# Kernel tuning notes

Hardware: AMD Instinct MI355X
Metric: run time of the kernel (lower is better)

The kernel has to match this reference:

```python
import jax, jax.numpy as jnp
import numpy as np

N_NODES = 100000
N_EDGES = 1600000
DIMS = [1, 20, 40, 60, 80, 100]  # int(k/5*qubo_size) for qubo_size=100


def setup_inputs() -> dict:
    key = jax.random.key(0)
    ks = jax.random.split(key, 16)
    inp = {
        "x": jax.random.normal(ks[0], (N_NODES, 1), dtype=jnp.float32),
        "edge_index": jax.random.randint(ks[1], (2, N_EDGES), 0, N_NODES, dtype=jnp.int64),
        "edge_weights": jax.random.uniform(ks[2], (N_EDGES,), dtype=jnp.float32),
    }
    for i in range(5):
        fan_in, fan_out = DIMS[i], DIMS[i + 1]
        scale = (2.0 / (fan_in + fan_out)) ** 0.5  # glorot-ish
        inp[f"W{i+1}"] = jax.random.normal(ks[3 + 2 * i], (fan_in, fan_out), dtype=jnp.float32) * scale
        inp[f"b{i+1}"] = jnp.zeros((fan_out,), dtype=jnp.float32)
    return inp


def reference(x, edge_index, edge_weights, W1, b1, W2, b2, W3, b3, W4, b4, W5, b5):
    n = x.shape[0]
    src, dst = edge_index[0], edge_index[1]
    # GCN symmetric normalization with self loops (fill value 1.0)
    deg = jax.ops.segment_sum(edge_weights, dst, num_segments=n) + 1.0
    dinv = jnp.where(deg > 0, deg ** -0.5, 0.0)
    norm = dinv[src] * edge_weights * dinv[dst]  # [E]
    self_norm = dinv * dinv                      # [N], self-loop weight 1

    def gcn_layer(h, W, b):
        h = h @ W  # [N, out]
        agg = jax.ops.segment_sum(h[src] * norm[:, None], dst, num_segments=n)
        agg = agg + h * self_norm[:, None]
        return agg + b

    for W, b in ((W1, b1), (W2, b2), (W3, b3), (W4, b4), (W5, b5)):
        x = gcn_layer(x, W, b)
    return jax.nn.relu(x)
```

## Files before the change

### kernel.cpp

```cpp
#include <hip/hip_runtime.h>


#define TBB 1024
#define TBK 512
#define BN 256
#define NBLK 256
#define STAGE 4096
#define CAP 4864

__device__ __forceinline__ void chains_block(
    const float* __restrict__ W1, const float* __restrict__ b1,
    const float* __restrict__ W2, const float* __restrict__ b2,
    const float* __restrict__ W3, const float* __restrict__ b3,
    const float* __restrict__ W4, const float* __restrict__ b4,
    const float* __restrict__ W5, float* __restrict__ coef,
    int* lflag, float (*A)[112], float (*Bm)[112]) {
    int t = threadIdx.x;
    if (t < 20) { A[0][t] = W1[t]; A[1][t] = b1[t]; }
    __syncthreads();
    if (t < 40) {
        for (int c = 0; c < 2; ++c) {
            float acc = 0.f;
            for (int k = 0; k < 20; ++k) acc += A[c][k] * W2[k * 40 + t];
            Bm[c][t] = acc;
        }
        Bm[2][t] = b2[t];
    }
    __syncthreads();
    if (t < 60) {
        for (int c = 0; c < 3; ++c) {
            float acc = 0.f;
            for (int k = 0; k < 40; ++k) acc += Bm[c][k] * W3[k * 60 + t];
            A[c][t] = acc;
        }
        A[3][t] = b3[t];
    }
    __syncthreads();
    if (t < 80) {
        for (int c = 0; c < 4; ++c) {
            float acc = 0.f;
            for (int k = 0; k < 60; ++k) acc += A[c][k] * W4[k * 80 + t];
            Bm[c][t] = acc;
        }
        Bm[4][t] = b4[t];
    }
    __syncthreads();
    if (t < 100) {
        int nz = 0;
        for (int c = 0; c < 5; ++c) {
            float acc = 0.f;
            for (int k = 0; k < 80; ++k) acc += Bm[c][k] * W5[k * 100 + t];
            coef[c * 100 + t] = acc;
            if (c > 0 && acc != 0.0f) nz = 1;
        }
        if (nz) atomicOr(lflag, 1);
    }
}

__global__ __launch_bounds__(TBB) void k_build(const int* __restrict__ src,
                                               const int* __restrict__ dst,
                                               const float* __restrict__ w,
                                               int* __restrict__ gcur,
                                               int2* __restrict__ payload,
                                               const float* __restrict__ W1, const float* __restrict__ b1,
                                               const float* __restrict__ W2, const float* __restrict__ b2,
                                               const float* __restrict__ W3, const float* __restrict__ b3,
                                               const float* __restrict__ W4, const float* __restrict__ b4,
                                               const float* __restrict__ W5, float* __restrict__ coef,
                                               int* __restrict__ uflag,
                                               int E, int B, int chunk) {
    __shared__ int lcur[512];
    __shared__ int lbase[512];
    __shared__ int goff[512];
    __shared__ int2 staged[STAGE];
    __shared__ unsigned short jbuf[STAGE];
    int blk = blockIdx.x, tid = threadIdx.x;
    if (blk == NBLK) {
        float (*A)[112]  = (float (*)[112])staged;
        float (*Bm)[112] = (float (*)[112])((char*)staged + 5 * 112 * 4);
        if (tid == 0) lcur[0] = 0;
        __syncthreads();
        chains_block(W1, b1, W2, b2, W3, b3, W4, b4, W5, coef, &lcur[0], A, Bm);
        __syncthreads();
        if (tid == 0) uflag[0] = lcur[0] ? 0 : 1;
        return;
    }
    int e0 = blk * chunk, e1 = min(E, e0 + chunk);
    for (int sbeg = e0; sbeg < e1; sbeg += STAGE) {
        int send = min(e1, sbeg + STAGE);
        int cnt = send - sbeg;
        if (tid < 512) lcur[tid] = 0;
        __syncthreads();
        int es[4], ed[4]; float ew[4]; int ne = 0;
        for (int i = sbeg + tid; i < send; i += TBB) {
            es[ne] = src[i]; ed[ne] = dst[i]; ew[ne] = w[i]; ++ne;
        }
        for (int k = 0; k < ne; ++k) atomicAdd(&lcur[ed[k] >> 8], 1);
        __syncthreads();
        int myv = (tid < 512) ? lcur[tid] : 0;
        if (tid < B && myv > 0)
            goff[tid] = atomicAdd(&gcur[tid], myv);
        if (tid < 512) lbase[tid] = myv;
        __syncthreads();
        for (int o = 1; o < 512; o <<= 1) {
            int t = (tid >= o && tid < 512) ? lbase[tid - o] : 0;
            __syncthreads();
            if (tid < 512) lbase[tid] += t;
            __syncthreads();
        }
        if (tid < 512) {
            int ex = lbase[tid] - myv;
            lbase[tid] = ex;
            lcur[tid] = ex;
        }
        __syncthreads();
        for (int k = 0; k < ne; ++k) {
            int j = ed[k] >> 8;
            int p = atomicAdd(&lcur[j], 1);
            staged[p] = make_int2(es[k] | ((ed[k] & 255) << 17), __float_as_int(ew[k]));
            jbuf[p] = (unsigned short)j;
        }
        __syncthreads();
        for (int p = tid; p < cnt; p += TBB) {
            int j = jbuf[p];
            int slot = goff[j] + (p - lbase[j]);
            if (slot < CAP) payload[(size_t)j * CAP + slot] = staged[p];
        }
        __syncthreads();
    }
}

__global__ __launch_bounds__(TBK) void k_bstats(const int* __restrict__ gcur,
                                                const int2* __restrict__ payload,
                                                const float* __restrict__ x,
                                                float* __restrict__ dinv,
                                                float* __restrict__ selfn,
                                                float2* __restrict__ q0, int n) {
    __shared__ float wdeg[BN];
    int j = blockIdx.x;
    int tid = threadIdx.x;
    if (tid < BN) wdeg[tid] = 0.f;
    __syncthreads();
    int len = min(gcur[j], CAP);
    const int2* row = payload + (size_t)j * CAP;
    for (int i = tid; i < len; i += TBK) {
        int2 p = row[i];
        atomicAdd(&wdeg[(p.x >> 17) & 255], __int_as_float(p.y));
    }
    __syncthreads();
    if (tid < BN) {
        int v = j * BN + tid;
        if (v < n) {
            float di = rsqrtf(wdeg[tid] + 1.0f);
            dinv[v] = di;
            selfn[v] = di * di;
            q0[v] = make_float2(di * x[v], di);
        }
    }
}

template <bool LAST>
__global__ __launch_bounds__(TBK) void k_pass(const int* __restrict__ gcur,
                                              const int2* __restrict__ payload,
                                              const float2* __restrict__ qin,
                                              const float* __restrict__ dinv,
                                              const float* __restrict__ selfn,
                                              const int* __restrict__ uflag,
                                              float2* __restrict__ qout,
                                              const float2* __restrict__ q1,
                                              const float2* __restrict__ q2,
                                              const float2* __restrict__ q3,
                                              const float* __restrict__ coef,
                                              const float* __restrict__ b5,
                                              float4* __restrict__ out, int n) {
    __shared__ float2 sacc[BN];
    int j = blockIdx.x;
    int tid = threadIdx.x;
    if (tid < BN) sacc[tid] = make_float2(0.f, 0.f);
    __syncthreads();
    const int skipy = uflag[0];
    int len = min(gcur[j], CAP);
    const int2* row = payload + (size_t)j * CAP;
    for (int i = tid; i < len; i += 2 * TBK) {
        int i2 = i + TBK;
        bool g2 = (i2 < len);
        int2 p1 = row[i];
        int2 p2 = g2 ? row[i2] : make_int2(0, 0);
        int s1 = p1.x & 0x1FFFF, s2 = p2.x & 0x1FFFF;
        if (LAST || skipy) {
            float qx1 = qin[s1].x;
            float qx2 = g2 ? qin[s2].x : 0.f;
            atomicAdd(&sacc[(p1.x >> 17) & 255].x, __int_as_float(p1.y) * qx1);
            if (g2) atomicAdd(&sacc[(p2.x >> 17) & 255].x, __int_as_float(p2.y) * qx2);
        } else {
            float2 qv1 = qin[s1];
            float2 qv2 = g2 ? qin[s2] : make_float2(0.f, 0.f);
            float w1 = __int_as_float(p1.y);
            int ld1 = (p1.x >> 17) & 255;
            atomicAdd(&sacc[ld1].x, w1 * qv1.x);
            atomicAdd(&sacc[ld1].y, w1 * qv1.y);
            if (g2) {
                float w2 = __int_as_float(p2.y);
                int ld2 = (p2.x >> 17) & 255;
                atomicAdd(&sacc[ld2].x, w2 * qv2.x);
                atomicAdd(&sacc[ld2].y, w2 * qv2.y);
            }
        }
    }
    __syncthreads();
    if constexpr (!LAST) {
        if (tid < BN) {
            int v = j * BN + tid;
            if (v < n) {
                float2 a = sacc[tid];
                float2 qv = qin[v];
                float sf = selfn[v];
                qout[v] = make_float2(sf * (a.x + qv.x), sf * (a.y + qv.y));
            }
        }
    } else {
        __shared__ float scoef[500];
        __shared__ float sb5[100];
        __shared__ float snode[BN * 5];
        for (int i = tid; i < 500; i += TBK) scoef[i] = coef[i];
        for (int i = tid; i < 100; i += TBK) sb5[i] = b5[i];
        if (tid < BN) {
            int v = j * BN + tid;
            if (v < n) {
                float2 qv = qin[v];
                float dv = dinv[v];
                float inv = 1.0f / dv;
                snode[tid * 5 + 0] = dv * (sacc[tid].x + qv.x);
                snode[tid * 5 + 1] = qv.y * inv;
                snode[tid * 5 + 2] = q3[v].y * inv;
                snode[tid * 5 + 3] = q2[v].y * inv;
                snode[tid * 5 + 4] = q1[v].y * inv;
            }
        }
        __syncthreads();
        int base_v = j * BN;
        int nv = min(BN, n - base_v);
        int total4 = nv * 25;
        for (int q = tid; q < total4; q += TBK) {
            int lv = q / 25;
            int col4 = q - lv * 25;
            int c0 = col4 * 4;
            float a5 = snode[lv * 5 + 0], u4 = snode[lv * 5 + 1], u3 = snode[lv * 5 + 2],
                  u2 = snode[lv * 5 + 3], u1 = snode[lv * 5 + 4];
            float4 r;
            float* rp = (float*)&r;
#pragma unroll
            for (int kk = 0; kk < 4; ++kk) {
                int c = c0 + kk;
                rp[kk] = fmaxf(sb5[c] + a5 * scoef[c] + u4 * scoef[100 + c] + u3 * scoef[200 + c]
                               + u2 * scoef[300 + c] + u1 * scoef[400 + c], 0.f);
            }
            out[(size_t)(base_v + lv) * 25 + col4] = r;
        }
    }
}


extern "C" void kernel_launch(void* const* d_in, const int* in_sizes, int n_in,
                              void* d_out, int out_size, void* d_ws, size_t ws_size,
                              hipStream_t stream) {
    const float* x  = (const float*)d_in[0];
    const int*   ei = (const int*)d_in[1];
    const float* w  = (const float*)d_in[2];
    const float* W1 = (const float*)d_in[3];  const float* b1 = (const float*)d_in[4];
    const float* W2 = (const float*)d_in[5];  const float* b2 = (const float*)d_in[6];
    const float* W3 = (const float*)d_in[7];  const float* b3 = (const float*)d_in[8];
    const float* W4 = (const float*)d_in[9];  const float* b4 = (const float*)d_in[10];
    const float* W5 = (const float*)d_in[11]; const float* b5 = (const float*)d_in[12];

    const int n = in_sizes[0];
    const int E = in_sizes[2];
    const int* src = ei;
    const int* dst = ei + E;

    const int B = (n + BN - 1) / BN;
    const int chunk = (E + NBLK - 1) / NBLK;

    char* ws = (char*)d_ws;
    size_t off = 0;
    auto alloc = [&](size_t bytes) -> void* {
        void* p = ws + off;
        off += (bytes + 255) & ~(size_t)255;
        return p;
    };
    int*   gcur    = (int*)alloc((size_t)B * 4);
    int*   uflag   = (int*)alloc(256);
    float* dinv    = (float*)alloc((size_t)n * 4);
    float* selfn   = (float*)alloc((size_t)n * 4);
    float* coef    = (float*)alloc(512 * 4);
    int2*  payload = (int2*)alloc((size_t)B * CAP * 8);
    float2* q[5];
    for (int i = 0; i < 5; ++i) q[i] = (float2*)alloc((size_t)n * 8);

    hipMemsetAsync(gcur, 0, (size_t)B * 4, stream);
    k_build<<<NBLK + 1, TBB, 0, stream>>>(src, dst, w, gcur, payload,
                                          W1, b1, W2, b2, W3, b3, W4, b4, W5, coef,
                                          uflag, E, B, chunk);
    k_bstats<<<B, TBK, 0, stream>>>(gcur, payload, x, dinv, selfn, q[0], n);

    for (int k = 1; k < 5; ++k)
        k_pass<false><<<B, TBK, 0, stream>>>(gcur, payload, q[k - 1], dinv, selfn, uflag, q[k],
                                             nullptr, nullptr, nullptr, nullptr, nullptr,
                                             nullptr, n);
    k_pass<true><<<B, TBK, 0, stream>>>(gcur, payload, q[4], dinv, selfn, uflag, nullptr,
                                        q[1], q[2], q[3], coef, b5, (float4*)d_out, n);
}
```

Baseline: 206.9 us.

## Split node state into SoA arrays and fold bucket-counter reset into build kernel

```diff
diff --git a/kernel.cpp b/kernel.cpp
--- a/kernel.cpp
+++ b/kernel.cpp
@@ -7,6 +7,7 @@
 #define NBLK 256
 #define STAGE 4096
 #define CAP 4864
+#define MAGIC 0x13572468
 
 __device__ __forceinline__ void chains_block(
     const float* __restrict__ W1, const float* __restrict__ b1,
@@ -61,6 +62,7 @@
                                                const int* __restrict__ dst,
                                                const float* __restrict__ w,
                                                int* __restrict__ gcur,
+                                               int* __restrict__ ready,
                                                int2* __restrict__ payload,
                                                const float* __restrict__ W1, const float* __restrict__ b1,
                                                const float* __restrict__ W2, const float* __restrict__ b2,
@@ -85,6 +87,12 @@
         if (tid == 0) uflag[0] = lcur[0] ? 0 : 1;
         return;
     }
+    if (blk == 0) {
+        for (int j2 = tid; j2 < B; j2 += TBB) gcur[j2] = 0;
+        __syncthreads();
+        if (tid == 0)
+            __hip_atomic_store(ready, MAGIC, __ATOMIC_RELEASE, __HIP_MEMORY_SCOPE_AGENT);
+    }
     int e0 = blk * chunk, e1 = min(E, e0 + chunk);
     for (int sbeg = e0; sbeg < e1; sbeg += STAGE) {
         int send = min(e1, sbeg + STAGE);
@@ -98,6 +106,10 @@
         for (int k = 0; k < ne; ++k) atomicAdd(&lcur[ed[k] >> 8], 1);
         __syncthreads();
         int myv = (tid < 512) ? lcur[tid] : 0;
+        if (sbeg == e0 && blk != 0 && tid < B) {
+            while (__hip_atomic_load(ready, __ATOMIC_ACQUIRE, __HIP_MEMORY_SCOPE_AGENT) != MAGIC)
+                __builtin_amdgcn_s_sleep(1);
+        }
         if (tid < B && myv > 0)
             goff[tid] = atomicAdd(&gcur[tid], myv);
         if (tid < 512) lbase[tid] = myv;
@@ -135,7 +147,8 @@
                                                 const float* __restrict__ x,
                                                 float* __restrict__ dinv,
                                                 float* __restrict__ selfn,
-                                                float2* __restrict__ q0, int n) {
+                                                float* __restrict__ qx0,
+                                                float* __restrict__ qy0, int n) {
     __shared__ float wdeg[BN];
     int j = blockIdx.x;
     int tid = threadIdx.x;
@@ -154,29 +167,25 @@
             float di = rsqrtf(wdeg[tid] + 1.0f);
             dinv[v] = di;
             selfn[v] = di * di;
-            q0[v] = make_float2(di * x[v], di);
-        }
-    }
-}
-
-template <bool LAST>
-__global__ __launch_bounds__(TBK) void k_pass(const int* __restrict__ gcur,
-                                              const int2* __restrict__ payload,
-                                              const float2* __restrict__ qin,
-                                              const float* __restrict__ dinv,
-                                              const float* __restrict__ selfn,
-                                              const int* __restrict__ uflag,
-                                              float2* __restrict__ qout,
-                                              const float2* __restrict__ q1,
-                                              const float2* __restrict__ q2,
-                                              const float2* __restrict__ q3,
-                                              const float* __restrict__ coef,
-                                              const float* __restrict__ b5,
-                                              float4* __restrict__ out, int n) {
-    __shared__ float2 sacc[BN];
+            qx0[v] = di * x[v];
+            qy0[v] = di;
+        }
+    }
+}
+
+__global__ __launch_bounds__(TBK) void k_mid(const int* __restrict__ gcur,
+                                             const int2* __restrict__ payload,
+                                             const float* __restrict__ qxin,
+                                             const float* __restrict__ qyin,
+                                             const float* __restrict__ selfn,
+                                             const int* __restrict__ uflag,
+                                             float* __restrict__ qxout,
+                                             float* __restrict__ qyout, int n) {
+    __shared__ float sacc_x[BN];
+    __shared__ float sacc_y[BN];
     int j = blockIdx.x;
     int tid = threadIdx.x;
-    if (tid < BN) sacc[tid] = make_float2(0.f, 0.f);
+    if (tid < BN) { sacc_x[tid] = 0.f; sacc_y[tid] = 0.f; }
     __syncthreads();
     const int skipy = uflag[0];
     int len = min(gcur[j], CAP);
@@ -187,76 +196,102 @@
         int2 p1 = row[i];
         int2 p2 = g2 ? row[i2] : make_int2(0, 0);
         int s1 = p1.x & 0x1FFFF, s2 = p2.x & 0x1FFFF;
-        if (LAST || skipy) {
-            float qx1 = qin[s1].x;
-            float qx2 = g2 ? qin[s2].x : 0.f;
-            atomicAdd(&sacc[(p1.x >> 17) & 255].x, __int_as_float(p1.y) * qx1);
-            if (g2) atomicAdd(&sacc[(p2.x >> 17) & 255].x, __int_as_float(p2.y) * qx2);
+        float w1 = __int_as_float(p1.y), w2 = __int_as_float(p2.y);
+        int ld1 = (p1.x >> 17) & 255, ld2 = (p2.x >> 17) & 255;
+        if (skipy) {
+            float qx1 = qxin[s1];
+            float qx2 = g2 ? qxin[s2] : 0.f;
+            atomicAdd(&sacc_x[ld1], w1 * qx1);
+            if (g2) atomicAdd(&sacc_x[ld2], w2 * qx2);
         } else {
-            float2 qv1 = qin[s1];
-            float2 qv2 = g2 ? qin[s2] : make_float2(0.f, 0.f);
-            float w1 = __int_as_float(p1.y);
-            int ld1 = (p1.x >> 17) & 255;
-            atomicAdd(&sacc[ld1].x, w1 * qv1.x);
-            atomicAdd(&sacc[ld1].y, w1 * qv1.y);
+            float qx1 = qxin[s1], qy1 = qyin[s1];
+            float qx2 = g2 ? qxin[s2] : 0.f, qy2 = g2 ? qyin[s2] : 0.f;
+            atomicAdd(&sacc_x[ld1], w1 * qx1);
+            atomicAdd(&sacc_y[ld1], w1 * qy1);
             if (g2) {
-                float w2 = __int_as_float(p2.y);
-                int ld2 = (p2.x >> 17) & 255;
-                atomicAdd(&sacc[ld2].x, w2 * qv2.x);
-                atomicAdd(&sacc[ld2].y, w2 * qv2.y);
+                atomicAdd(&sacc_x[ld2], w2 * qx2);
+                atomicAdd(&sacc_y[ld2], w2 * qy2);
             }
         }
     }
     __syncthreads();
-    if constexpr (!LAST) {
-        if (tid < BN) {
-            int v = j * BN + tid;
-            if (v < n) {
-                float2 a = sacc[tid];
-                float2 qv = qin[v];
-                float sf = selfn[v];
-                qout[v] = make_float2(sf * (a.x + qv.x), sf * (a.y + qv.y));
-            }
-        }
-    } else {
-        __shared__ float scoef[500];
-        __shared__ float sb5[100];
-        __shared__ float snode[BN * 5];
-        for (int i = tid; i < 500; i += TBK) scoef[i] = coef[i];
-        for (int i = tid; i < 100; i += TBK) sb5[i] = b5[i];
-        if (tid < BN) {
-            int v = j * BN + tid;
-            if (v < n) {
-                float2 qv = qin[v];
-                float dv = dinv[v];
-                float inv = 1.0f / dv;
-                snode[tid * 5 + 0] = dv * (sacc[tid].x + qv.x);
-                snode[tid * 5 + 1] = qv.y * inv;
-                snode[tid * 5 + 2] = q3[v].y * inv;
-                snode[tid * 5 + 3] = q2[v].y * inv;
-                snode[tid * 5 + 4] = q1[v].y * inv;
-            }
-        }
-        __syncthreads();
-        int base_v = j * BN;
-        int nv = min(BN, n - base_v);
-        int total4 = nv * 25;
-        for (int q = tid; q < total4; q += TBK) {
-            int lv = q / 25;
-            int col4 = q - lv * 25;
-            int c0 = col4 * 4;
-            float a5 = snode[lv * 5 + 0], u4 = snode[lv * 5 + 1], u3 = snode[lv * 5 + 2],
-                  u2 = snode[lv * 5 + 3], u1 = snode[lv * 5 + 4];
-            float4 r;
-            float* rp = (float*)&r;
+    if (tid < BN) {
+        int v = j * BN + tid;
+        if (v < n) {
+            float sf = selfn[v];
+            qxout[v] = sf * (sacc_x[tid] + qxin[v]);
+            if (!skipy) qyout[v] = sf * (sacc_y[tid] + qyin[v]);
+        }
+    }
+}
+
+__global__ __launch_bounds__(TBK) void k_last(const int* __restrict__ gcur,
+                                              const int2* __restrict__ payload,
+                                              const float* __restrict__ qx4,
+                                              const float* __restrict__ qy1,
+                                              const float* __restrict__ qy2,
+                                              const float* __restrict__ qy3,
+                                              const float* __restrict__ qy4,
+                                              const float* __restrict__ dinv,
+                                              const int* __restrict__ uflag,
+                                              const float* __restrict__ coef,
+                                              const float* __restrict__ b5,
+                                              float4* __restrict__ out, int n) {
+    __shared__ float sacc_x[BN];
+    __shared__ float scoef[500];
+    __shared__ float sb5[100];
+    __shared__ float snode[BN * 5];
+    int j = blockIdx.x;
+    int tid = threadIdx.x;
+    if (tid < BN) sacc_x[tid] = 0.f;
+    for (int i = tid; i < 500; i += TBK) scoef[i] = coef[i];
+    for (int i = tid; i < 100; i += TBK) sb5[i] = b5[i];
+    __syncthreads();
+    const int skipy = uflag[0];
+    int len = min(gcur[j], CAP);
+    const int2* row = payload + (size_t)j * CAP;
+    for (int i = tid; i < len; i += 2 * TBK) {
+        int i2 = i + TBK;
+        bool g2 = (i2 < len);
+        int2 p1 = row[i];
+        int2 p2 = g2 ? row[i2] : make_int2(0, 0);
+        float qx1 = qx4[p1.x & 0x1FFFF];
+        float qx2 = g2 ? qx4[p2.x & 0x1FFFF] : 0.f;
+        atomicAdd(&sacc_x[(p1.x >> 17) & 255], __int_as_float(p1.y) * qx1);
+        if (g2) atomicAdd(&sacc_x[(p2.x >> 17) & 255], __int_as_float(p2.y) * qx2);
+    }
+    __syncthreads();
+    if (tid < BN) {
+        int v = j * BN + tid;
+        if (v < n) {
+            float dv = dinv[v];
+            float inv = 1.0f / dv;
+            snode[tid * 5 + 0] = dv * (sacc_x[tid] + qx4[v]);
+            snode[tid * 5 + 1] = skipy ? 0.f : qy4[v] * inv;
+            snode[tid * 5 + 2] = skipy ? 0.f : qy3[v] * inv;
+            snode[tid * 5 + 3] = skipy ? 0.f : qy2[v] * inv;
+            snode[tid * 5 + 4] = skipy ? 0.f : qy1[v] * inv;
+        }
+    }
+    __syncthreads();
+    int base_v = j * BN;
+    int nv = min(BN, n - base_v);
+    int total4 = nv * 25;
+    for (int q = tid; q < total4; q += TBK) {
+        int lv = q / 25;
+        int col4 = q - lv * 25;
+        int c0 = col4 * 4;
+        float a5 = snode[lv * 5 + 0], u4 = snode[lv * 5 + 1], u3 = snode[lv * 5 + 2],
+              u2 = snode[lv * 5 + 3], u1 = snode[lv * 5 + 4];
+        float4 r;
+        float* rp = (float*)&r;
 #pragma unroll
-            for (int kk = 0; kk < 4; ++kk) {
-                int c = c0 + kk;
-                rp[kk] = fmaxf(sb5[c] + a5 * scoef[c] + u4 * scoef[100 + c] + u3 * scoef[200 + c]
-                               + u2 * scoef[300 + c] + u1 * scoef[400 + c], 0.f);
-            }
-            out[(size_t)(base_v + lv) * 25 + col4] = r;
-        }
+        for (int kk = 0; kk < 4; ++kk) {
+            int c = c0 + kk;
+            rp[kk] = fmaxf(sb5[c] + a5 * scoef[c] + u4 * scoef[100 + c] + u3 * scoef[200 + c]
+                           + u2 * scoef[300 + c] + u1 * scoef[400 + c], 0.f);
+        }
+        out[(size_t)(base_v + lv) * 25 + col4] = r;
     }
 }
 
@@ -289,24 +324,25 @@
         return p;
     };
     int*   gcur    = (int*)alloc((size_t)B * 4);
+    int*   ready   = (int*)alloc(256);
     int*   uflag   = (int*)alloc(256);
     float* dinv    = (float*)alloc((size_t)n * 4);
     float* selfn   = (float*)alloc((size_t)n * 4);
     float* coef    = (float*)alloc(512 * 4);
     int2*  payload = (int2*)alloc((size_t)B * CAP * 8);
-    float2* q[5];
-    for (int i = 0; i < 5; ++i) q[i] = (float2*)alloc((size_t)n * 8);
-
-    hipMemsetAsync(gcur, 0, (size_t)B * 4, stream);
-    k_build<<<NBLK + 1, TBB, 0, stream>>>(src, dst, w, gcur, payload,
+    float* qx[5];
+    float* qy[5];
+    for (int i = 0; i < 5; ++i) qx[i] = (float*)alloc((size_t)n * 4);
+    for (int i = 0; i < 5; ++i) qy[i] = (float*)alloc((size_t)n * 4);
+
+    k_build<<<NBLK + 1, TBB, 0, stream>>>(src, dst, w, gcur, ready, payload,
                                           W1, b1, W2, b2, W3, b3, W4, b4, W5, coef,
                                           uflag, E, B, chunk);
-    k_bstats<<<B, TBK, 0, stream>>>(gcur, payload, x, dinv, selfn, q[0], n);
+    k_bstats<<<B, TBK, 0, stream>>>(gcur, payload, x, dinv, selfn, qx[0], qy[0], n);
 
     for (int k = 1; k < 5; ++k)
-        k_pass<false><<<B, TBK, 0, stream>>>(gcur, payload, q[k - 1], dinv, selfn, uflag, q[k],
-                                             nullptr, nullptr, nullptr, nullptr, nullptr,
-                                             nullptr, n);
-    k_pass<true><<<B, TBK, 0, stream>>>(gcur, payload, q[4], dinv, selfn, uflag, nullptr,
-                                        q[1], q[2], q[3], coef, b5, (float4*)d_out, n);
-}
+        k_mid<<<B, TBK, 0, stream>>>(gcur, payload, qx[k - 1], qy[k - 1], selfn, uflag,
+                                     qx[k], qy[k], n);
+    k_last<<<B, TBK, 0, stream>>>(gcur, payload, qx[4], qy[1], qy[2], qy[3], qy[4],
+                                  dinv, uflag, coef, b5, (float4*)d_out, n);
+}
```

Measured after the change: 207.6 us. About the same (+0.3%).
